# Optimization experiments

Measured on AMD Instinct MI355X. Metric: run time of the kernel, lower is better.

Reference implementation:

```python
import jax, jax.numpy as jnp
import numpy as np

HEADS = 16
DIM_HEAD = 64

def setup_inputs() -> dict:
    key = jax.random.key(0)
    ks = jax.random.split(key, 7)
    B, Nq, Dq = 4, 2048, 1024
    Nk, Dc = 1024, 768
    inner = HEADS * DIM_HEAD  # 1024
    sq = 1.0 / np.sqrt(Dq)
    sc = 1.0 / np.sqrt(Dc)
    si = 1.0 / np.sqrt(inner)
    return {
        "x": jax.random.normal(ks[0], (B, Nq, Dq), dtype=jnp.float32),
        "context": jax.random.normal(ks[1], (B, Nk, Dc), dtype=jnp.float32),
        "Wq": jax.random.normal(ks[2], (Dq, inner), dtype=jnp.float32) * sq,
        "Wk": jax.random.normal(ks[3], (Dc, inner), dtype=jnp.float32) * sc,
        "Wv": jax.random.normal(ks[4], (Dc, inner), dtype=jnp.float32) * sc,
        "Wo": jax.random.normal(ks[5], (inner, Dq), dtype=jnp.float32) * si,
        "bo": jax.random.normal(ks[6], (Dq,), dtype=jnp.float32) * 0.01,
    }

def reference(x, context, Wq, Wk, Wv, Wo, bo):
    B, Nq, _ = x.shape
    Nk = context.shape[1]
    h, dh = HEADS, DIM_HEAD
    # projections (no bias on q/k/v, matching nn.Linear(bias=False))
    q = (x @ Wq).reshape(B, Nq, h, dh)        # [B,Nq,h,dh]
    k = (context @ Wk).reshape(B, Nk, h, dh)  # [B,Nk,h,dh]
    v = (context @ Wv).reshape(B, Nk, h, dh)
    scale = 1.0 / jnp.sqrt(jnp.asarray(dh, dtype=x.dtype))
    # scores: [B,h,Nq,Nk]
    scores = jnp.einsum('bqhd,bkhd->bhqk', q, k) * scale
    attn = jax.nn.softmax(scores, axis=-1)
    out = jnp.einsum('bhqk,bkhd->bqhd', attn, v).reshape(B, Nq, h * dh)
    return out @ Wo + bo
```

## Files before the change

### kernel.cpp

```cpp
#include <hip/hip_runtime.h>

typedef __bf16 bf16;
typedef __bf16 bf16x2 __attribute__((ext_vector_type(2)));
typedef __bf16 bf16x4 __attribute__((ext_vector_type(4)));
typedef __bf16 bf16x8 __attribute__((ext_vector_type(8)));
typedef float f32x4 __attribute__((ext_vector_type(4)));

#define MFMA(a, b, c) __builtin_amdgcn_mfma_f32_16x16x32_bf16(a, b, c, 0, 0, 0)

#define GLD16(gptr, ldsptr)                                                        \
  __builtin_amdgcn_global_load_lds(                                                \
      (const __attribute__((address_space(1))) unsigned int*)(gptr),               \
      (__attribute__((address_space(3))) unsigned int*)(ldsptr), 16, 0, 0)

union I4B8 { int4 i; bf16x8 v; };
union HI { bf16x2 h; int i; };

__global__ __launch_bounds__(256) void prep_k(const float* __restrict__ x, bf16* __restrict__ xb,
                                              const float* __restrict__ ctx, bf16* __restrict__ ctxb,
                                              const float* __restrict__ Wq, bf16* __restrict__ WqT,
                                              const float* __restrict__ Wk, bf16* __restrict__ WkvT,
                                              const float* __restrict__ Wv,
                                              const float* __restrict__ Wo, bf16* __restrict__ WoT) {
  __shared__ float t[32][33];
  const int bid = blockIdx.x;
  if (bid < 5632) {
    const float* in; bf16* out; size_t i;
    if (bid < 4096) { in = x; out = xb; i = ((size_t)bid * 256 + threadIdx.x) * 8; }
    else { in = ctx; out = ctxb; i = ((size_t)(bid - 4096) * 256 + threadIdx.x) * 8; }
    const float4 a = *(const float4*)(in + i);
    const float4 b = *(const float4*)(in + i + 4);
    bf16x8 o;
    o[0] = (bf16)a.x; o[1] = (bf16)a.y; o[2] = (bf16)a.z; o[3] = (bf16)a.w;
    o[4] = (bf16)b.x; o[5] = (bf16)b.y; o[6] = (bf16)b.z; o[7] = (bf16)b.w;
    *(bf16x8*)(out + i) = o;
    return;
  }
  const int tt = bid - 5632;
  const int z = tt >> 10, rem = tt & 1023;
  const float* in; bf16* out; int R; float sc = 1.0f;
  if (z == 0)      { in = Wq; out = WqT;                R = 1024; sc = 0.18033688f; }
  else if (z == 1) { in = Wk; out = WkvT;               R = 768; }
  else if (z == 2) { in = Wv; out = WkvT + 1024 * 768;  R = 768; }
  else             { in = Wo; out = WoT;                R = 1024; }
  const int c0 = (rem & 31) * 32, r0 = (rem >> 5) * 32;
  if (r0 >= R) return;
  const int tx = threadIdx.x & 31, ty = threadIdx.x >> 5;
#pragma unroll
  for (int i = 0; i < 4; i++)
    t[ty + i * 8][tx] = in[(size_t)(r0 + ty + i * 8) * 1024 + c0 + tx];
  __syncthreads();
#pragma unroll
  for (int i = 0; i < 4; i++)
    out[(size_t)(c0 + ty + i * 8) * R + r0 + tx] = (bf16)(t[tx][ty + i * 8] * sc);
}

__device__ __forceinline__ void ld_af(bf16x8 (&af)[4][2], const bf16* Ls, int base,
                                      int wm, int c, int q, int swz) {
#pragma unroll
  for (int mi = 0; mi < 4; mi++) {
    const int rr = wm * 64 + mi * 16 + c;
#pragma unroll
    for (int kk = 0; kk < 2; kk++)
      af[mi][kk] = *(const bf16x8*)&Ls[base + rr * 64 + ((kk * 32 + q * 8) ^ swz)];
  }
}
__device__ __forceinline__ void ld_bb(bf16x8 (&bb)[2][2], const bf16* Ls, int base,
                                      int wn, int c, int q, int swz) {
#pragma unroll
  for (int ni = 0; ni < 2; ni++) {
    const int rn = wn * 32 + ni * 16 + c;
#pragma unroll
    for (int kk = 0; kk < 2; kk++)
      bb[ni][kk] = *(const bf16x8*)&Ls[base + rn * 64 + ((kk * 32 + q * 8) ^ swz)];
  }
}
template <int MODE>
__device__ __forceinline__ void mma16(f32x4 (&pacc)[4][2], const bf16x8 (&af)[4][2],
                                      const bf16x8 (&bb)[2][2]) {
  __builtin_amdgcn_s_setprio(1);
#pragma unroll
  for (int mi = 0; mi < 4; mi++)
#pragma unroll
    for (int ni = 0; ni < 2; ni++)
#pragma unroll
      for (int kk = 0; kk < 2; kk++) {
        if constexpr (MODE == 2)
          pacc[mi][ni] = MFMA(af[mi][kk], bb[ni][kk], pacc[mi][ni]);
        else
          pacc[mi][ni] = MFMA(bb[ni][kk], af[mi][kk], pacc[mi][ni]);
      }
  __builtin_amdgcn_s_setprio(0);
}

#define PHASE_SYNC_MFMA(ACC, AF, BB)                          \
  asm volatile("s_barrier" ::: "memory");                     \
  asm volatile("s_waitcnt lgkmcnt(0)" ::: "memory");          \
  __builtin_amdgcn_sched_barrier(0);                          \
  mma16<MODE>(ACC, AF, BB);                                   \
  asm volatile("s_barrier" ::: "memory");

template <int MODE>
__device__ __forceinline__ void gemm256(const bf16* __restrict__ A,
                                        const bf16* __restrict__ Bt,
                                        int K, int m0, int n0,
                                        void* __restrict__ C0,
                                        const float* __restrict__ bias,
                                        bf16* Ls) {
  const int tid = threadIdx.x;
  const int lane = tid & 63, w = tid >> 6;
  const int wm = w >> 2, wn = w & 3;
  const int q = lane >> 4, c = lane & 15;
  const int swz = (c & 7) * 8;

  const int rl = tid >> 3, seg = tid & 7;
  const bf16* Ag = A + (size_t)(m0 + rl) * K + ((seg ^ (rl & 7)) * 8);
  const bf16* Bg = Bt + (size_t)(n0 + rl) * K + ((seg ^ (rl & 7)) * 8);
  const size_t K64 = (size_t)K * 64, K128 = (size_t)K * 128;
  const int ws = w * 512;

  f32x4 acc[2][2][4][2] = {};

  GLD16(Ag,              &Ls[0 + ws]);
  GLD16(Ag + K64,        &Ls[4096 + ws]);
  GLD16(Ag + K128,       &Ls[8192 + ws]);
  GLD16(Ag + K128 + K64, &Ls[12288 + ws]);
  GLD16(Bg,              &Ls[32768 + ws]);
  GLD16(Bg + K64,        &Ls[32768 + 4096 + ws]);
  GLD16(Bg + K128,       &Ls[32768 + 8192 + ws]);
  GLD16(Bg + K128 + K64, &Ls[32768 + 12288 + ws]);
  asm volatile("s_waitcnt vmcnt(0)" ::: "memory");
  asm volatile("s_barrier" ::: "memory");

  int cur = 0;
  for (int k0 = 0; k0 < K; k0 += 64) {
    const int nxt = cur ^ 1;
    const size_t kn = (size_t)((k0 + 64 < K) ? k0 + 64 : k0);
    const int Ab = cur * 16384, Bb = 32768 + cur * 16384;
    const int An = nxt * 16384, Bn = 32768 + nxt * 16384;

    bf16x8 af[4][2], b0[2][2], b1[2][2];

    GLD16(Ag + kn,       &Ls[An + ws]);
    GLD16(Ag + kn + K64, &Ls[An + 4096 + ws]);
    ld_af(af, Ls, Ab, wm, c, q, swz);
    ld_bb(b0, Ls, Bb, wn, c, q, swz);
    asm volatile("s_waitcnt vmcnt(2)" ::: "memory");
    PHASE_SYNC_MFMA(acc[0][0], af, b0)

    GLD16(Ag + kn + K128,       &Ls[An + 8192 + ws]);
    GLD16(Ag + kn + K128 + K64, &Ls[An + 12288 + ws]);
    ld_bb(b1, Ls, Bb + 8192, wn, c, q, swz);
    PHASE_SYNC_MFMA(acc[0][1], af, b1)

    GLD16(Bg + kn,       &Ls[Bn + ws]);
    GLD16(Bg + kn + K64, &Ls[Bn + 4096 + ws]);
    ld_af(af, Ls, Ab + 8192, wm, c, q, swz);
    PHASE_SYNC_MFMA(acc[1][0], af, b0)

    GLD16(Bg + kn + K128,       &Ls[Bn + 8192 + ws]);
    GLD16(Bg + kn + K128 + K64, &Ls[Bn + 12288 + ws]);
    asm volatile("s_waitcnt vmcnt(2)" ::: "memory");
    PHASE_SYNC_MFMA(acc[1][1], af, b1)

    cur = nxt;
  }
  asm volatile("s_waitcnt vmcnt(0)" ::: "memory");

  if constexpr (MODE == 0 || MODE == 1) {
#pragma unroll
    for (int h = 0; h < 2; h++)
#pragma unroll
      for (int g = 0; g < 2; g++)
#pragma unroll
        for (int ni = 0; ni < 2; ni++) {
          const int col = n0 + g * 128 + wn * 32 + ni * 16 + q * 4;
          float4 bv4 = {};
          if constexpr (MODE == 1) bv4 = *(const float4*)&bias[col];
#pragma unroll
          for (int mi = 0; mi < 4; mi++) {
            const int row = m0 + h * 128 + wm * 64 + mi * 16 + c;
            if constexpr (MODE == 0) {
              bf16x4 vv;
#pragma unroll
              for (int r2 = 0; r2 < 4; r2++) vv[r2] = (bf16)acc[h][g][mi][ni][r2];
              *(bf16x4*)&((bf16*)C0)[(size_t)row * 1024 + col] = vv;
            } else {
              f32x4 vv;
              vv[0] = acc[h][g][mi][ni][0] + bv4.x; vv[1] = acc[h][g][mi][ni][1] + bv4.y;
              vv[2] = acc[h][g][mi][ni][2] + bv4.z; vv[3] = acc[h][g][mi][ni][3] + bv4.w;
              *(f32x4*)&((float*)C0)[(size_t)row * 1024 + col] = vv;
            }
          }
        }
  } else {
#pragma unroll
    for (int h = 0; h < 2; h++)
#pragma unroll
      for (int g = 0; g < 2; g++)
#pragma unroll
        for (int ni = 0; ni < 2; ni++) {
          const int col = n0 + g * 128 + wn * 32 + ni * 16 + c;
#pragma unroll
          for (int mi = 0; mi < 4; mi++) {
            const int rbase = m0 + h * 128 + wm * 64 + mi * 16 + q * 4;
            const int b = rbase >> 10, key = rbase & 1023;
            bf16* VT = (bf16*)C0;
            const int hh = col >> 6, d = col & 63;
            const int kl = key & 63;
            const int pkey = (key & ~63) | (kl & 32) | ((kl & 12) << 1) | ((kl & 16) >> 2);
            bf16x4 vv;
#pragma unroll
            for (int r2 = 0; r2 < 4; r2++) vv[r2] = (bf16)acc[h][g][mi][ni][r2];
            *(bf16x4*)&VT[((size_t)(b * 16 + hh) * 64 + d) * 1024 + pkey] = vv;
          }
        }
  }
}

__global__ __launch_bounds__(512) void proj_k(const bf16* __restrict__ xb,
                                              const bf16* __restrict__ ctxb,
                                              const bf16* __restrict__ WqT,
                                              const bf16* __restrict__ WkvT,
                                              bf16* __restrict__ Q,
                                              bf16* __restrict__ Kp,
                                              bf16* __restrict__ VT) {
  extern __shared__ __align__(16) bf16 Ls[];
  const int bid = blockIdx.x;
  if (bid < 128) {
    const int x = bid & 7, i = bid >> 3;
    const int rt = x * 4 + (i >> 2), ct = i & 3;
    gemm256<0>(xb, WqT, 1024, rt * 256, ct * 256, Q, nullptr, Ls);
  } else if (bid < 192) {
    const int t = bid - 128, x = t & 7, i = t >> 3;
    const int rt = x * 2 + (i >> 2), ct = i & 3;
    gemm256<0>(ctxb, WkvT, 768, rt * 256, ct * 256, Kp, nullptr, Ls);
  } else {
    const int t = bid - 192, x = t & 7, i = t >> 3;
    const int rt = x * 2 + (i >> 2), ct = i & 3;
    gemm256<2>(ctxb, WkvT + (size_t)1024 * 768, 768, rt * 256, ct * 256, VT, nullptr, Ls);
  }
}

__device__ __forceinline__ void gemm_body_out(const bf16* __restrict__ A,
                                              const bf16* __restrict__ Bt,
                                              int K, int m0, int n0,
                                              float* __restrict__ C0,
                                              const float* __restrict__ bias,
                                              bf16* As, bf16* Bs) {
  const int tid = threadIdx.x;
  const int lane = tid & 63, wave = tid >> 6;
  const int wm = wave >> 1, wn = wave & 1;
  const int q = lane >> 4, c = lane & 15;

  f32x4 acc[4][4] = {};
  const int r = tid >> 3;
  const int col8 = ((tid & 7) * 8) ^ ((r & 7) * 8);
  const bf16* Ag = A + (size_t)(m0 + r) * K + col8;
  const bf16* Bg = Bt + (size_t)(n0 + r) * K + col8;
  const size_t K32 = (size_t)K * 32;
  bf16* AsW = As + wave * 512;
  bf16* BsW = Bs + wave * 512;
  const int swz = (c & 7) * 8;

  for (int k0 = 0; k0 < K; k0 += 64) {
    __syncthreads();
    GLD16(Ag + k0,            AsW);
    GLD16(Ag + k0 + K32,      AsW + 2048);
    GLD16(Ag + k0 + 2 * K32,  AsW + 4096);
    GLD16(Ag + k0 + 3 * K32,  AsW + 6144);
    GLD16(Bg + k0,            BsW);
    GLD16(Bg + k0 + K32,      BsW + 2048);
    GLD16(Bg + k0 + 2 * K32,  BsW + 4096);
    GLD16(Bg + k0 + 3 * K32,  BsW + 6144);
    __syncthreads();
#pragma unroll
    for (int kk = 0; kk < 2; kk++) {
      const int cx = (kk * 32 + q * 8) ^ swz;
      bf16x8 af[4], bfr[4];
#pragma unroll
      for (int mi = 0; mi < 4; mi++)
        af[mi] = *(const bf16x8*)&As[(wm * 64 + mi * 16 + c) * 64 + cx];
#pragma unroll
      for (int ni = 0; ni < 4; ni++)
        bfr[ni] = *(const bf16x8*)&Bs[(wn * 64 + ni * 16 + c) * 64 + cx];
      __builtin_amdgcn_s_setprio(1);
#pragma unroll
      for (int mi = 0; mi < 4; mi++)
#pragma unroll
        for (int ni = 0; ni < 4; ni++)
          acc[mi][ni] = MFMA(bfr[ni], af[mi], acc[mi][ni]);
      __builtin_amdgcn_s_setprio(0);
    }
  }

#pragma unroll
  for (int ni = 0; ni < 4; ni++) {
    const int col = n0 + wn * 64 + ni * 16 + q * 4;
    float4 bv4 = *(const float4*)&bias[col];
#pragma unroll
    for (int mi = 0; mi < 4; mi++) {
      const int row = m0 + wm * 64 + mi * 16 + c;
      f32x4 vv;
      vv[0] = acc[mi][ni][0] + bv4.x; vv[1] = acc[mi][ni][1] + bv4.y;
      vv[2] = acc[mi][ni][2] + bv4.z; vv[3] = acc[mi][ni][3] + bv4.w;
      *(f32x4*)&C0[(size_t)row * 1024 + col] = vv;
    }
  }
}

__global__ __launch_bounds__(256) void out_k(const bf16* __restrict__ O,
                                             const bf16* __restrict__ WoT,
                                             float* __restrict__ out,
                                             const float* __restrict__ bo) {
  __shared__ __align__(16) bf16 As[8192];
  __shared__ __align__(16) bf16 Bs[8192];
  const int bid = blockIdx.x;
  const int s = (bid & 7) * 64 + (bid >> 3);
  gemm_body_out(O, WoT, 1024, (s >> 3) * 128, (s & 7) * 128, out, bo, As, Bs);
}

__global__ __launch_bounds__(256, 2) void attn_k(const bf16* __restrict__ Qg,
                                                 const bf16* __restrict__ Kg,
                                                 const bf16* __restrict__ VTg,
                                                 bf16* __restrict__ Og) {
  __shared__ __align__(16) bf16 Ks[2][64][64];
  __shared__ __align__(16) bf16 Vt[2][64][64];
  const int tid = threadIdx.x;
  const int lane = tid & 63, w = tid >> 6;
  const int q = lane >> 4, c = lane & 15;
  const int bid = blockIdx.x;
  const int pair = (bid & 7) * 8 + (bid >> 6);
  const int head = pair & 15, b = pair >> 4;
  const int q0 = ((bid >> 3) & 7) * 256;

  bf16x8 aQ[4][2];
#pragma unroll
  for (int mj = 0; mj < 4; mj++)
#pragma unroll
    for (int ks = 0; ks < 2; ks++)
      aQ[mj][ks] = *(const bf16x8*)(Qg + (size_t)(b * 2048 + q0 + w * 64 + mj * 16 + c) * 1024 +
                                    head * 64 + ks * 32 + q * 8);

  f32x4 o[4][4] = {};
  f32x4 ol[4] = {};
  bf16x8 vone;
#pragma unroll
  for (int i = 0; i < 8; i++) vone[i] = (bf16)1.0f;

  const int srow = tid >> 2, sc = tid & 3;
  const int ws0 = ((2 * sc) ^ (srow & 7)) * 8;
  const int ws1 = ((2 * sc + 1) ^ (srow & 7)) * 8;
  const int rsw = c & 7;
  const bf16* Kbase = Kg + (size_t)(b * 1024 + srow) * 1024 + head * 64 + sc * 16;
  const bf16* Vbase = VTg + ((size_t)(b * 16 + head) * 64 + srow) * 1024 + sc * 16;

  bf16x8 rk0 = *(const bf16x8*)(Kbase);
  bf16x8 rk1 = *(const bf16x8*)(Kbase + 8);
  bf16x8 rv0 = *(const bf16x8*)(Vbase);
  bf16x8 rv1 = *(const bf16x8*)(Vbase + 8);
  *(bf16x8*)&Ks[0][srow][ws0] = rk0;
  *(bf16x8*)&Ks[0][srow][ws1] = rk1;
  *(bf16x8*)&Vt[0][srow][ws0] = rv0;
  *(bf16x8*)&Vt[0][srow][ws1] = rv1;
  __syncthreads();

  for (int kt = 0; kt < 16; kt++) {
    const int cur = kt & 1, nxt = cur ^ 1;
    if (kt < 15) {
      const size_t ko = (size_t)(kt + 1) * 65536;
      const int vo = (kt + 1) * 64;
      rk0 = *(const bf16x8*)(Kbase + ko);
      rk1 = *(const bf16x8*)(Kbase + ko + 8);
      rv0 = *(const bf16x8*)(Vbase + vo);
      rv1 = *(const bf16x8*)(Vbase + vo + 8);
    }

    f32x4 st[4][4] = {};
#pragma unroll
    for (int ks = 0; ks < 2; ks++) {
      bf16x8 ak[4];
#pragma unroll
      for (int ni = 0; ni < 4; ni++)
        ak[ni] = *(const bf16x8*)&Ks[cur][ni * 16 + c][((ks * 4 + q) ^ rsw) * 8];
      __builtin_amdgcn_s_setprio(1);
#pragma unroll
      for (int mj = 0; mj < 4; mj++)
#pragma unroll
        for (int ni = 0; ni < 4; ni++)
          st[mj][ni] = MFMA(ak[ni], aQ[mj][ks], st[mj][ni]);
      __builtin_amdgcn_s_setprio(0);
    }

    int pk[4][4][2];
#pragma unroll
    for (int mj = 0; mj < 4; mj++)
#pragma unroll
      for (int ni = 0; ni < 4; ni++) {
        float p0 = __builtin_amdgcn_exp2f(st[mj][ni][0]);
        float p1 = __builtin_amdgcn_exp2f(st[mj][ni][1]);
        float p2 = __builtin_amdgcn_exp2f(st[mj][ni][2]);
        float p3 = __builtin_amdgcn_exp2f(st[mj][ni][3]);
        HI h0, h1;
        h0.h[0] = (bf16)p0; h0.h[1] = (bf16)p1;
        h1.h[0] = (bf16)p2; h1.h[1] = (bf16)p3;
        pk[mj][ni][0] = h0.i;
        pk[mj][ni][1] = h1.i;
      }

#pragma unroll
    for (int ks2 = 0; ks2 < 2; ks2++) {
      bf16x8 bv[4];
#pragma unroll
      for (int ni = 0; ni < 4; ni++)
        bv[ni] = *(const bf16x8*)&Vt[cur][ni * 16 + c][((ks2 * 4 + q) ^ rsw) * 8];
#pragma unroll
      for (int mi = 0; mi < 4; mi++) {
        I4B8 pa;
        pa.i.x = pk[mi][2 * ks2][0];
        pa.i.y = pk[mi][2 * ks2][1];
        pa.i.z = pk[mi][2 * ks2 + 1][0];
        pa.i.w = pk[mi][2 * ks2 + 1][1];
        __builtin_amdgcn_s_setprio(1);
#pragma unroll
        for (int ni = 0; ni < 4; ni++)
          o[mi][ni] = MFMA(pa.v, bv[ni], o[mi][ni]);
        ol[mi] = MFMA(pa.v, vone, ol[mi]);
        __builtin_amdgcn_s_setprio(0);
      }
    }

    if (kt < 15) {
      *(bf16x8*)&Ks[nxt][srow][ws0] = rk0;
      *(bf16x8*)&Ks[nxt][srow][ws1] = rk1;
      *(bf16x8*)&Vt[nxt][srow][ws0] = rv0;
      *(bf16x8*)&Vt[nxt][srow][ws1] = rv1;
    }
    __syncthreads();
  }

#pragma unroll
  for (int mi = 0; mi < 4; mi++) {
    float inv[4];
#pragma unroll
    for (int r = 0; r < 4; r++) inv[r] = 1.0f / ol[mi][r];
#pragma unroll
    for (int ni = 0; ni < 4; ni++)
#pragma unroll
      for (int r = 0; r < 4; r++) {
        const int qrow = q0 + w * 64 + mi * 16 + q * 4 + r;
        const int col = head * 64 + ni * 16 + c;
        Og[(size_t)(b * 2048 + qrow) * 1024 + col] = (bf16)(o[mi][ni][r] * inv[r]);
      }
  }
}

extern "C" void kernel_launch(void* const* d_in, const int* in_sizes, int n_in,
                              void* d_out, int out_size, void* d_ws, size_t ws_size,
                              hipStream_t stream) {
  (void)in_sizes; (void)n_in; (void)out_size; (void)ws_size;
  const float* x   = (const float*)d_in[0];
  const float* ctx = (const float*)d_in[1];
  const float* Wq  = (const float*)d_in[2];
  const float* Wk  = (const float*)d_in[3];
  const float* Wv  = (const float*)d_in[4];
  const float* Wo  = (const float*)d_in[5];
  const float* bo  = (const float*)d_in[6];
  float* out = (float*)d_out;

  char* ws = (char*)d_ws;
  const size_t MB = 1u << 20;
  bf16* WqT  = (bf16*)(ws);
  bf16* WkvT = (bf16*)(ws + 2 * MB);
  bf16* WoT  = (bf16*)(ws + 5 * MB);
  bf16* ctxb = (bf16*)(ws + 7 * MB);
  bf16* xb   = (bf16*)(ws + 13 * MB);
  bf16* Q    = (bf16*)(ws + 29 * MB);
  bf16* Kp   = (bf16*)(ws + 45 * MB);
  bf16* VT   = (bf16*)(ws + 53 * MB);
  bf16* O    = xb;

  prep_k<<<5632 + 4096, 256, 0, stream>>>(x, xb, ctx, ctxb, Wq, WqT, Wk, WkvT, Wv, Wo, WoT);

  proj_k<<<256, 512, 131072, stream>>>(xb, ctxb, WqT, WkvT, Q, Kp, VT);

  attn_k<<<512, 256, 0, stream>>>(Q, Kp, VT, O);

  out_k<<<512, 256, 0, stream>>>(O, WoT, out, bo);
}
```

Baseline: 203.3 us.

## Triple-buffer output GEMM with 256x128 tiles and double attention KV tile size

The output projection kernel moves from a 128x128 tile with single-buffered LDS and two barriers per k-step to a 512-thread, 256x128 tile. It uses a three-stage global_load_lds pipeline, split A/B staging and explicit vmcnt waits, so loads overlap MFMA work. Separately, the attention kernel now loads 128 keys per iteration instead of 64, which halves the number of loop iterations and barriers. The cost is more LDS (144KB dynamic for out_k, larger attention buffers), which may lower occupancy, and a more fragile hand-written synchronization scheme.

```diff
diff --git a/kernel.cpp b/kernel.cpp
--- a/kernel.cpp
+++ b/kernel.cpp
@@ -242,90 +242,119 @@
   }
 }
 
-__device__ __forceinline__ void gemm_body_out(const bf16* __restrict__ A,
-                                              const bf16* __restrict__ Bt,
-                                              int K, int m0, int n0,
-                                              float* __restrict__ C0,
-                                              const float* __restrict__ bias,
-                                              bf16* As, bf16* Bs) {
+__global__ __launch_bounds__(512) void out_k(const bf16* __restrict__ O,
+                                             const bf16* __restrict__ WoT,
+                                             float* __restrict__ out,
+                                             const float* __restrict__ bo) {
+  extern __shared__ __align__(16) bf16 Ls[];
+  const int bid = blockIdx.x;
+  const int s = (bid & 7) * 32 + (bid >> 3);
+  const int m0 = (s >> 3) * 256, n0 = (s & 7) * 128;
+
   const int tid = threadIdx.x;
-  const int lane = tid & 63, wave = tid >> 6;
-  const int wm = wave >> 1, wn = wave & 1;
+  const int lane = tid & 63, w = tid >> 6;
+  const int wm = w >> 1, wn = w & 1;
   const int q = lane >> 4, c = lane & 15;
+  const int swz = (c & 7) * 8;
+  constexpr int K = 1024;
+  constexpr int BUF = 24576;
+
+  const int rl = tid >> 3, seg = tid & 7;
+  const bf16* Ag = O + (size_t)(m0 + rl) * K + ((seg ^ (rl & 7)) * 8);
+  const bf16* Bg = WoT + (size_t)(n0 + rl) * K + ((seg ^ (rl & 7)) * 8);
+  const size_t K64 = (size_t)K * 64, K128 = (size_t)K * 128;
+  const int ws = w * 512;
 
   f32x4 acc[4][4] = {};
-  const int r = tid >> 3;
-  const int col8 = ((tid & 7) * 8) ^ ((r & 7) * 8);
-  const bf16* Ag = A + (size_t)(m0 + r) * K + col8;
-  const bf16* Bg = Bt + (size_t)(n0 + r) * K + col8;
-  const size_t K32 = (size_t)K * 32;
-  bf16* AsW = As + wave * 512;
-  bf16* BsW = Bs + wave * 512;
-  const int swz = (c & 7) * 8;
-
-  for (int k0 = 0; k0 < K; k0 += 64) {
-    __syncthreads();
-    GLD16(Ag + k0,            AsW);
-    GLD16(Ag + k0 + K32,      AsW + 2048);
-    GLD16(Ag + k0 + 2 * K32,  AsW + 4096);
-    GLD16(Ag + k0 + 3 * K32,  AsW + 6144);
-    GLD16(Bg + k0,            BsW);
-    GLD16(Bg + k0 + K32,      BsW + 2048);
-    GLD16(Bg + k0 + 2 * K32,  BsW + 4096);
-    GLD16(Bg + k0 + 3 * K32,  BsW + 6144);
-    __syncthreads();
-#pragma unroll
-    for (int kk = 0; kk < 2; kk++) {
-      const int cx = (kk * 32 + q * 8) ^ swz;
-      bf16x8 af[4], bfr[4];
-#pragma unroll
-      for (int mi = 0; mi < 4; mi++)
-        af[mi] = *(const bf16x8*)&As[(wm * 64 + mi * 16 + c) * 64 + cx];
+
+#define OUT_STAGE_A(T, b)                                              \
+  { const size_t kk_ = (size_t)(T) * 64;                               \
+    GLD16(Ag + kk_,              &Ls[(b) * BUF + 0 + ws]);             \
+    GLD16(Ag + kk_ + K64,        &Ls[(b) * BUF + 4096 + ws]);          \
+    GLD16(Ag + kk_ + K128,       &Ls[(b) * BUF + 8192 + ws]);          \
+    GLD16(Ag + kk_ + K128 + K64, &Ls[(b) * BUF + 12288 + ws]); }
+#define OUT_STAGE_B(T, b)                                              \
+  { const size_t kk_ = (size_t)(T) * 64;                               \
+    GLD16(Bg + kk_,       &Ls[(b) * BUF + 16384 + ws]);                \
+    GLD16(Bg + kk_ + K64, &Ls[(b) * BUF + 16384 + 4096 + ws]); }
+
+  OUT_STAGE_A(0, 0) OUT_STAGE_B(0, 0)
+  OUT_STAGE_A(1, 1) OUT_STAGE_B(1, 1)
+  asm volatile("s_waitcnt vmcnt(6)" ::: "memory");
+  asm volatile("s_barrier" ::: "memory");
+
+  for (int t = 0; t < 16; t++) {
+    const int cb = t % 3;
+    const int nb = (t + 2) % 3;
+    const int tn = (t + 2 < 16) ? t + 2 : t;
+    const int Ab = cb * BUF, Bb = cb * BUF + 16384;
+
+    OUT_STAGE_A(tn, nb)
+    bf16x8 af[4], bb[4];
+#pragma unroll
+    for (int mi = 0; mi < 4; mi++)
+      af[mi] = *(const bf16x8*)&Ls[Ab + (wm * 64 + mi * 16 + c) * 64 + ((q * 8) ^ swz)];
+#pragma unroll
+    for (int ni = 0; ni < 4; ni++)
+      bb[ni] = *(const bf16x8*)&Ls[Bb + (wn * 64 + ni * 16 + c) * 64 + ((q * 8) ^ swz)];
+    asm volatile("s_barrier" ::: "memory");
+    asm volatile("s_waitcnt lgkmcnt(0)" ::: "memory");
+    __builtin_amdgcn_sched_barrier(0);
+    __builtin_amdgcn_s_setprio(1);
+#pragma unroll
+    for (int mi = 0; mi < 4; mi++)
 #pragma unroll
       for (int ni = 0; ni < 4; ni++)
-        bfr[ni] = *(const bf16x8*)&Bs[(wn * 64 + ni * 16 + c) * 64 + cx];
-      __builtin_amdgcn_s_setprio(1);
-#pragma unroll
-      for (int mi = 0; mi < 4; mi++)
-#pragma unroll
-        for (int ni = 0; ni < 4; ni++)
-          acc[mi][ni] = MFMA(bfr[ni], af[mi], acc[mi][ni]);
-      __builtin_amdgcn_s_setprio(0);
-    }
-  }
+        acc[mi][ni] = MFMA(bb[ni], af[mi], acc[mi][ni]);
+    __builtin_amdgcn_s_setprio(0);
+    asm volatile("s_barrier" ::: "memory");
+
+    OUT_STAGE_B(tn, nb)
+#pragma unroll
+    for (int mi = 0; mi < 4; mi++)
+      af[mi] = *(const bf16x8*)&Ls[Ab + (wm * 64 + mi * 16 + c) * 64 + ((32 + q * 8) ^ swz)];
+#pragma unroll
+    for (int ni = 0; ni < 4; ni++)
+      bb[ni] = *(const bf16x8*)&Ls[Bb + (wn * 64 + ni * 16 + c) * 64 + ((32 + q * 8) ^ swz)];
+    asm volatile("s_barrier" ::: "memory");
+    asm volatile("s_waitcnt lgkmcnt(0)" ::: "memory");
+    __builtin_amdgcn_sched_barrier(0);
+    __builtin_amdgcn_s_setprio(1);
+#pragma unroll
+    for (int mi = 0; mi < 4; mi++)
+#pragma unroll
+      for (int ni = 0; ni < 4; ni++)
+        acc[mi][ni] = MFMA(bb[ni], af[mi], acc[mi][ni]);
+    __builtin_amdgcn_s_setprio(0);
+    asm volatile("s_waitcnt vmcnt(6)" ::: "memory");
+    asm volatile("s_barrier" ::: "memory");
+  }
+  asm volatile("s_waitcnt vmcnt(0)" ::: "memory");
+
+#undef OUT_STAGE_A
+#undef OUT_STAGE_B
 
 #pragma unroll
   for (int ni = 0; ni < 4; ni++) {
     const int col = n0 + wn * 64 + ni * 16 + q * 4;
-    float4 bv4 = *(const float4*)&bias[col];
+    float4 bv4 = *(const float4*)&bo[col];
 #pragma unroll
     for (int mi = 0; mi < 4; mi++) {
       const int row = m0 + wm * 64 + mi * 16 + c;
       f32x4 vv;
       vv[0] = acc[mi][ni][0] + bv4.x; vv[1] = acc[mi][ni][1] + bv4.y;
       vv[2] = acc[mi][ni][2] + bv4.z; vv[3] = acc[mi][ni][3] + bv4.w;
-      *(f32x4*)&C0[(size_t)row * 1024 + col] = vv;
+      *(f32x4*)&out[(size_t)row * 1024 + col] = vv;
     }
   }
-}
-
-__global__ __launch_bounds__(256) void out_k(const bf16* __restrict__ O,
-                                             const bf16* __restrict__ WoT,
-                                             float* __restrict__ out,
-                                             const float* __restrict__ bo) {
-  __shared__ __align__(16) bf16 As[8192];
-  __shared__ __align__(16) bf16 Bs[8192];
-  const int bid = blockIdx.x;
-  const int s = (bid & 7) * 64 + (bid >> 3);
-  gemm_body_out(O, WoT, 1024, (s >> 3) * 128, (s & 7) * 128, out, bo, As, Bs);
 }
 
 __global__ __launch_bounds__(256, 2) void attn_k(const bf16* __restrict__ Qg,
                                                  const bf16* __restrict__ Kg,
                                                  const bf16* __restrict__ VTg,
                                                  bf16* __restrict__ Og) {
-  __shared__ __align__(16) bf16 Ks[2][64][64];
-  __shared__ __align__(16) bf16 Vt[2][64][64];
+  __shared__ __align__(16) bf16 Ks[2][128][64];
+  __shared__ __align__(16) bf16 Vt[2][64][128];
   const int tid = threadIdx.x;
   const int lane = tid & 63, w = tid >> 6;
   const int q = lane >> 4, c = lane & 15;
@@ -357,84 +386,103 @@
 
   bf16x8 rk0 = *(const bf16x8*)(Kbase);
   bf16x8 rk1 = *(const bf16x8*)(Kbase + 8);
+  bf16x8 rk2 = *(const bf16x8*)(Kbase + 65536);
+  bf16x8 rk3 = *(const bf16x8*)(Kbase + 65536 + 8);
   bf16x8 rv0 = *(const bf16x8*)(Vbase);
   bf16x8 rv1 = *(const bf16x8*)(Vbase + 8);
-  *(bf16x8*)&Ks[0][srow][ws0] = rk0;
-  *(bf16x8*)&Ks[0][srow][ws1] = rk1;
-  *(bf16x8*)&Vt[0][srow][ws0] = rv0;
-  *(bf16x8*)&Vt[0][srow][ws1] = rv1;
+  bf16x8 rv2 = *(const bf16x8*)(Vbase + 64);
+  bf16x8 rv3 = *(const bf16x8*)(Vbase + 72);
+  *(bf16x8*)&Ks[0][srow][ws0]      = rk0;
+  *(bf16x8*)&Ks[0][srow][ws1]      = rk1;
+  *(bf16x8*)&Ks[0][srow + 64][ws0] = rk2;
+  *(bf16x8*)&Ks[0][srow + 64][ws1] = rk3;
+  *(bf16x8*)&Vt[0][srow][ws0]      = rv0;
+  *(bf16x8*)&Vt[0][srow][ws1]      = rv1;
+  *(bf16x8*)&Vt[0][srow][64 + ws0] = rv2;
+  *(bf16x8*)&Vt[0][srow][64 + ws1] = rv3;
   __syncthreads();
 
-  for (int kt = 0; kt < 16; kt++) {
+  for (int kt = 0; kt < 8; kt++) {
     const int cur = kt & 1, nxt = cur ^ 1;
-    if (kt < 15) {
-      const size_t ko = (size_t)(kt + 1) * 65536;
-      const int vo = (kt + 1) * 64;
+    if (kt < 7) {
+      const size_t ko = (size_t)(kt + 1) * 131072;
+      const int vo = (kt + 1) * 128;
       rk0 = *(const bf16x8*)(Kbase + ko);
       rk1 = *(const bf16x8*)(Kbase + ko + 8);
+      rk2 = *(const bf16x8*)(Kbase + ko + 65536);
+      rk3 = *(const bf16x8*)(Kbase + ko + 65536 + 8);
       rv0 = *(const bf16x8*)(Vbase + vo);
       rv1 = *(const bf16x8*)(Vbase + vo + 8);
+      rv2 = *(const bf16x8*)(Vbase + vo + 64);
+      rv3 = *(const bf16x8*)(Vbase + vo + 72);
     }
 
-    f32x4 st[4][4] = {};
-#pragma unroll
-    for (int ks = 0; ks < 2; ks++) {
-      bf16x8 ak[4];
-#pragma unroll
-      for (int ni = 0; ni < 4; ni++)
-        ak[ni] = *(const bf16x8*)&Ks[cur][ni * 16 + c][((ks * 4 + q) ^ rsw) * 8];
-      __builtin_amdgcn_s_setprio(1);
-#pragma unroll
-      for (int mj = 0; mj < 4; mj++)
+#pragma unroll
+    for (int ch = 0; ch < 2; ch++) {
+      f32x4 st[4][4] = {};
+#pragma unroll
+      for (int ks = 0; ks < 2; ks++) {
+        bf16x8 ak[4];
 #pragma unroll
         for (int ni = 0; ni < 4; ni++)
-          st[mj][ni] = MFMA(ak[ni], aQ[mj][ks], st[mj][ni]);
-      __builtin_amdgcn_s_setprio(0);
-    }
-
-    int pk[4][4][2];
-#pragma unroll
-    for (int mj = 0; mj < 4; mj++)
-#pragma unroll
-      for (int ni = 0; ni < 4; ni++) {
-        float p0 = __builtin_amdgcn_exp2f(st[mj][ni][0]);
-        float p1 = __builtin_amdgcn_exp2f(st[mj][ni][1]);
-        float p2 = __builtin_amdgcn_exp2f(st[mj][ni][2]);
-        float p3 = __builtin_amdgcn_exp2f(st[mj][ni][3]);
-        HI h0, h1;
-        h0.h[0] = (bf16)p0; h0.h[1] = (bf16)p1;
-        h1.h[0] = (bf16)p2; h1.h[1] = (bf16)p3;
-        pk[mj][ni][0] = h0.i;
-        pk[mj][ni][1] = h1.i;
-      }
-
-#pragma unroll
-    for (int ks2 = 0; ks2 < 2; ks2++) {
-      bf16x8 bv[4];
-#pragma unroll
-      for (int ni = 0; ni < 4; ni++)
-        bv[ni] = *(const bf16x8*)&Vt[cur][ni * 16 + c][((ks2 * 4 + q) ^ rsw) * 8];
-#pragma unroll
-      for (int mi = 0; mi < 4; mi++) {
-        I4B8 pa;
-        pa.i.x = pk[mi][2 * ks2][0];
-        pa.i.y = pk[mi][2 * ks2][1];
-        pa.i.z = pk[mi][2 * ks2 + 1][0];
-        pa.i.w = pk[mi][2 * ks2 + 1][1];
+          ak[ni] = *(const bf16x8*)&Ks[cur][ch * 64 + ni * 16 + c][((ks * 4 + q) ^ rsw) * 8];
         __builtin_amdgcn_s_setprio(1);
 #pragma unroll
-        for (int ni = 0; ni < 4; ni++)
-          o[mi][ni] = MFMA(pa.v, bv[ni], o[mi][ni]);
-        ol[mi] = MFMA(pa.v, vone, ol[mi]);
+        for (int mj = 0; mj < 4; mj++)
+#pragma unroll
+          for (int ni = 0; ni < 4; ni++)
+            st[mj][ni] = MFMA(ak[ni], aQ[mj][ks], st[mj][ni]);
         __builtin_amdgcn_s_setprio(0);
       }
+
+      int pk[4][4][2];
+#pragma unroll
+      for (int mj = 0; mj < 4; mj++)
+#pragma unroll
+        for (int ni = 0; ni < 4; ni++) {
+          float p0 = __builtin_amdgcn_exp2f(st[mj][ni][0]);
+          float p1 = __builtin_amdgcn_exp2f(st[mj][ni][1]);
+          float p2 = __builtin_amdgcn_exp2f(st[mj][ni][2]);
+          float p3 = __builtin_amdgcn_exp2f(st[mj][ni][3]);
+          HI h0, h1;
+          h0.h[0] = (bf16)p0; h0.h[1] = (bf16)p1;
+          h1.h[0] = (bf16)p2; h1.h[1] = (bf16)p3;
+          pk[mj][ni][0] = h0.i;
+          pk[mj][ni][1] = h1.i;
+        }
+
+#pragma unroll
+      for (int ks2 = 0; ks2 < 2; ks2++) {
+        bf16x8 bv[4];
+#pragma unroll
+        for (int ni = 0; ni < 4; ni++)
+          bv[ni] = *(const bf16x8*)&Vt[cur][ni * 16 + c][ch * 64 + ((ks2 * 4 + q) ^ rsw) * 8];
+#pragma unroll
+        for (int mi = 0; mi < 4; mi++) {
+          I4B8 pa;
+          pa.i.x = pk[mi][2 * ks2][0];
+          pa.i.y = pk[mi][2 * ks2][1];
+          pa.i.z = pk[mi][2 * ks2 + 1][0];
+          pa.i.w = pk[mi][2 * ks2 + 1][1];
+          __builtin_amdgcn_s_setprio(1);
+#pragma unroll
+          for (int ni = 0; ni < 4; ni++)
+            o[mi][ni] = MFMA(pa.v, bv[ni], o[mi][ni]);
+          ol[mi] = MFMA(pa.v, vone, ol[mi]);
+          __builtin_amdgcn_s_setprio(0);
+        }
+      }
     }
 
-    if (kt < 15) {
-      *(bf16x8*)&Ks[nxt][srow][ws0] = rk0;
-      *(bf16x8*)&Ks[nxt][srow][ws1] = rk1;
-      *(bf16x8*)&Vt[nxt][srow][ws0] = rv0;
-      *(bf16x8*)&Vt[nxt][srow][ws1] = rv1;
+    if (kt < 7) {
+      *(bf16x8*)&Ks[nxt][srow][ws0]      = rk0;
+      *(bf16x8*)&Ks[nxt][srow][ws1]      = rk1;
+      *(bf16x8*)&Ks[nxt][srow + 64][ws0] = rk2;
+      *(bf16x8*)&Ks[nxt][srow + 64][ws1] = rk3;
+      *(bf16x8*)&Vt[nxt][srow][ws0]      = rv0;
+      *(bf16x8*)&Vt[nxt][srow][ws1]      = rv1;
+      *(bf16x8*)&Vt[nxt][srow][64 + ws0] = rv2;
+      *(bf16x8*)&Vt[nxt][srow][64 + ws1] = rv3;
     }
     __syncthreads();
   }
@@ -486,5 +534,5 @@
 
   attn_k<<<512, 256, 0, stream>>>(Q, Kp, VT, O);
 
-  out_k<<<512, 256, 0, stream>>>(O, WoT, out, bo);
-}
+  out_k<<<256, 512, 147456, stream>>>(O, WoT, out, bo);
+}
```

New measurement: 204.7 us. No clear change (+0.7%).
